# Optimization experiments

Hardware: AMD Instinct MI355X
Metric: run time of the kernel (lower is better)

## Reference

```python
import jax, jax.numpy as jnp
import numpy as np

B, C, F, T = 4, 64, 256, 256
CH = C // 2  # self.n_ch inside the module
EPS = 1e-5


def _cbp(x, W, b, g, be, m, v, a):
    # 1x1 conv == channel matmul, then BatchNorm (inference stats) + PReLU (scalar slope)
    y = jnp.einsum('oi,bift->boft', W, x) + b[None, :, None, None]
    y = (y - m[None, :, None, None]) * jax.lax.rsqrt(v[None, :, None, None] + EPS)
    y = y * g[None, :, None, None] + be[None, :, None, None]
    return jnp.where(y > 0, y, a * y)


def setup_inputs() -> dict:
    key = jax.random.key(0)
    ks = jax.random.split(key, 16)

    def conv_params(i, cin, cout, pre):
        W = jax.random.normal(ks[i], (cout, cin), dtype=jnp.float32) * 0.05
        return {
            pre + '_W': W,
            pre + '_b': jnp.zeros((cout,), jnp.float32),
            pre + '_g': jnp.ones((cout,), jnp.float32),
            pre + '_be': jnp.zeros((cout,), jnp.float32),
            pre + '_m': jax.random.normal(ks[i + 1], (cout,), dtype=jnp.float32) * 0.1,
            pre + '_v': jax.random.uniform(ks[i + 2], (cout,), dtype=jnp.float32) + 0.5,
            pre + '_a': jnp.float32(0.25),
        }

    d = {
        'inp': jax.random.normal(ks[12], (B, C, F, T), dtype=jnp.float32),
        'x': jax.random.normal(ks[13], (B, C, F, T), dtype=jnp.float32),
    }
    d.update(conv_params(0, C, 2 * CH, 'fqk'))
    d.update(conv_params(3, C, CH, 'fv'))
    d.update(conv_params(6, C, 2 * CH, 'tqk'))
    d.update(conv_params(9, CH, C, 'proj'))
    return d


def reference(inp, x,
              fqk_W, fqk_b, fqk_g, fqk_be, fqk_m, fqk_v, fqk_a,
              fv_W, fv_b, fv_g, fv_be, fv_m, fv_v, fv_a,
              tqk_W, tqk_b, tqk_g, tqk_be, tqk_m, tqk_v, tqk_a,
              proj_W, proj_b, proj_g, proj_be, proj_m, proj_v, proj_a):
    scale = 1.0 / jnp.sqrt(jnp.float32(CH))

    # frequency attention
    f_qk = _cbp(inp, fqk_W, fqk_b, fqk_g, fqk_be, fqk_m, fqk_v, fqk_a)  # B,2CH,F,T
    vf = _cbp(x, fv_W, fv_b, fv_g, fv_be, fv_m, fv_v, fv_a)             # B,CH,F,T
    r = f_qk.reshape(f_qk.shape[0], CH, 2, F, T)  # 'b (c k) f t -> b c k f t'
    qf, kf = r[:, :, 0], r[:, :, 1]
    f_score = jnp.einsum('bcft,bcyt->btfy', qf, kf) * scale
    f_score = jax.nn.softmax(f_score, axis=-1)
    fout = jnp.einsum('btfy,bcyt->bcft', f_score, vf)

    # time attention (causal mask)
    t_qk = _cbp(inp, tqk_W, tqk_b, tqk_g, tqk_be, tqk_m, tqk_v, tqk_a)
    r = t_qk.reshape(t_qk.shape[0], CH, 2, F, T)
    qt, kt = r[:, :, 0], r[:, :, 1]
    t_score = jnp.einsum('bcft,bcfy->bfty', qt, kt) * scale
    mask = jnp.triu(jnp.ones((T, T), dtype=bool), k=1)  # j - i + 1 with i == j
    neg = -jnp.finfo(t_score.dtype).max
    t_score = jnp.where(mask, neg, t_score)
    t_score = jax.nn.softmax(t_score, axis=-1)
    tout = jnp.einsum('bfty,bcfy->bcft', t_score, fout)

    out = _cbp(tout, proj_W, proj_b, proj_g, proj_be, proj_m, proj_v, proj_a)
    return out + x
```

## Files before the change

kernel.cpp:

```cpp
#include <hip/hip_runtime.h>
#include <hip/hip_bf16.h>

typedef __hip_bfloat16 bf16;
typedef __attribute__((ext_vector_type(8))) short bf16x8;
typedef __attribute__((ext_vector_type(4))) float f32x4;
typedef __attribute__((ext_vector_type(8))) unsigned short u16x8;
typedef __attribute__((ext_vector_type(4))) unsigned int u32x4;
typedef __attribute__((ext_vector_type(2))) unsigned int u32x2;

struct ConvP {
  const float* W; const float* bi; const float* g; const float* be;
  const float* m; const float* v; const float* a;
};

__device__ __forceinline__ unsigned short f2bf(float f) {
  __hip_bfloat16 h = __float2bfloat16(f);
  return __builtin_bit_cast(unsigned short, h);
}
__device__ __forceinline__ float bf2f(unsigned short u) {
  return __uint_as_float(((unsigned)u) << 16);
}

__global__ __launch_bounds__(256, 2) void conv_qkv(
    const float* __restrict__ inp, const float* __restrict__ x,
    ConvP fqk, ConvP fv, ConvP tqk,
    bf16* __restrict__ Qf, bf16* __restrict__ Kf, bf16* __restrict__ Vf,
    bf16* __restrict__ Qt, bf16* __restrict__ Kt)
{
  __shared__ __attribute__((aligned(16))) unsigned short Xb[64 * 260];
  __shared__ __attribute__((aligned(16))) unsigned short S0[256 * 40];
  __shared__ __attribute__((aligned(16))) unsigned short S1[256 * 40];
  __shared__ __attribute__((aligned(8)))  float2 Pc[160];

  const int tid = threadIdx.x;
  const int b = blockIdx.x >> 8;
  const int f = blockIdx.x & 255;
  const size_t gbase = (size_t)b * 64 * 65536 + f * 256;
  const size_t tbase = (size_t)(b * 256 + f) * 8192;

  const int lane = tid & 63;
  const int wid = tid >> 6;
  const int m16 = lane & 15;
  const int quad = lane >> 4;

  if (tid < 160) {
    const ConvP& P = (tid < 64) ? fqk : (tid < 128) ? tqk : fv;
    const int o = (tid < 64) ? tid : (tid < 128) ? tid - 64 : tid - 128;
    const float A = P.g[o] * rsqrtf(P.v[o] + 1e-5f);
    const float B2 = (P.bi[o] - P.m[o]) * A + P.be[o];
    Pc[tid] = make_float2(A, B2);
  }

  auto load_X = [&](const float* __restrict__ src) {
    #pragma unroll
    for (int r = 0; r < 16; ++r) {
      const int idx = r * 256 + tid;
      const int c = idx >> 6;
      const int t0 = (idx & 63) * 4;
      const float4 v = *(const float4*)(src + gbase + (size_t)c * 65536 + t0);
      unsigned lo = (unsigned)f2bf(v.x) | (((unsigned)f2bf(v.y)) << 16);
      unsigned hi = (unsigned)f2bf(v.z) | (((unsigned)f2bf(v.w)) << 16);
      u32x2 pk = {lo, hi};
      *(u32x2*)&Xb[c * 260 + t0] = pk;
    }
  };

  auto load_A = [&](const float* __restrict__ W, int rowbase, int ks) {
    const float* p = W + (rowbase + m16) * 64 + ks * 32 + quad * 8;
    const float4 lo = *(const float4*)p;
    const float4 hi = *(const float4*)(p + 4);
    bf16x8 r;
    r[0] = (short)f2bf(lo.x); r[1] = (short)f2bf(lo.y);
    r[2] = (short)f2bf(lo.z); r[3] = (short)f2bf(lo.w);
    r[4] = (short)f2bf(hi.x); r[5] = (short)f2bf(hi.y);
    r[6] = (short)f2bf(hi.z); r[7] = (short)f2bf(hi.w);
    return r;
  };

  auto load_B = [&](int tt, int ks) {
    const int t = tt * 16 + m16;
    const int i0 = ks * 32 + quad * 8;
    bf16x8 r;
    #pragma unroll
    for (int j = 0; j < 8; ++j) r[j] = (short)Xb[(i0 + j) * 260 + t];
    return r;
  };

  auto emit = [&](const unsigned short* S, bf16* __restrict__ dst) {
    #pragma unroll
    for (int r = 0; r < 4; ++r) {
      const int chunk = r * 256 + tid;
      const int t = chunk >> 2, part = chunk & 3;
      u32x4 v = *(const u32x4*)&S[t * 40 + part * 8];
      *(u32x4*)(dst + tbase + (size_t)chunk * 8) = v;
    }
  };

  auto leaky = [](float y, float alpha) { return y > 0.f ? y : alpha * y; };

  auto qk_pass = [&](const ConvP& P, int pcb) {
    bf16x8 A[4][2];
    #pragma unroll
    for (int ot = 0; ot < 4; ++ot)
      #pragma unroll
      for (int ks = 0; ks < 2; ++ks) A[ot][ks] = load_A(P.W, ot * 16, ks);
    float pA[4][4], pB[4][4];
    #pragma unroll
    for (int ot = 0; ot < 4; ++ot)
      #pragma unroll
      for (int r = 0; r < 4; ++r) {
        const float2 pp = Pc[pcb + ot * 16 + quad * 4 + r];
        pA[ot][r] = pp.x; pB[ot][r] = pp.y;
      }
    const float alpha = P.a[0];
    #pragma unroll
    for (int i = 0; i < 4; ++i) {
      const int tt = wid * 4 + i;
      const bf16x8 B0 = load_B(tt, 0);
      const bf16x8 B1 = load_B(tt, 1);
      const int t = tt * 16 + m16;
      #pragma unroll
      for (int ot = 0; ot < 4; ++ot) {
        f32x4 acc = {0.f, 0.f, 0.f, 0.f};
        acc = __builtin_amdgcn_mfma_f32_16x16x32_bf16(A[ot][0], B0, acc, 0, 0, 0);
        acc = __builtin_amdgcn_mfma_f32_16x16x32_bf16(A[ot][1], B1, acc, 0, 0, 0);
        float y[4];
        #pragma unroll
        for (int r = 0; r < 4; ++r)
          y[r] = leaky(acc[r] * pA[ot][r] + pB[ot][r], alpha);
        const int ch0 = ot * 8 + quad * 2;
        unsigned q = (unsigned)f2bf(y[0]) | (((unsigned)f2bf(y[2])) << 16);
        unsigned k = (unsigned)f2bf(y[1]) | (((unsigned)f2bf(y[3])) << 16);
        *(unsigned*)&S0[t * 40 + ch0] = q;
        *(unsigned*)&S1[t * 40 + ch0] = k;
      }
    }
  };

  auto v_pass = [&]() {
    bf16x8 A[2][2];
    #pragma unroll
    for (int ot = 0; ot < 2; ++ot)
      #pragma unroll
      for (int ks = 0; ks < 2; ++ks) A[ot][ks] = load_A(fv.W, ot * 16, ks);
    float pA[2][4], pB[2][4];
    #pragma unroll
    for (int ot = 0; ot < 2; ++ot)
      #pragma unroll
      for (int r = 0; r < 4; ++r) {
        const float2 pp = Pc[128 + ot * 16 + quad * 4 + r];
        pA[ot][r] = pp.x; pB[ot][r] = pp.y;
      }
    const float alpha = fv.a[0];
    #pragma unroll
    for (int i = 0; i < 4; ++i) {
      const int tt = wid * 4 + i;
      const bf16x8 B0 = load_B(tt, 0);
      const bf16x8 B1 = load_B(tt, 1);
      const int t = tt * 16 + m16;
      #pragma unroll
      for (int ot = 0; ot < 2; ++ot) {
        f32x4 acc = {0.f, 0.f, 0.f, 0.f};
        acc = __builtin_amdgcn_mfma_f32_16x16x32_bf16(A[ot][0], B0, acc, 0, 0, 0);
        acc = __builtin_amdgcn_mfma_f32_16x16x32_bf16(A[ot][1], B1, acc, 0, 0, 0);
        float y[4];
        #pragma unroll
        for (int r = 0; r < 4; ++r)
          y[r] = leaky(acc[r] * pA[ot][r] + pB[ot][r], alpha);
        const int ch = ot * 16 + quad * 4;
        *(unsigned*)&S0[t * 40 + ch]     = (unsigned)f2bf(y[0]) | (((unsigned)f2bf(y[1])) << 16);
        *(unsigned*)&S0[t * 40 + ch + 2] = (unsigned)f2bf(y[2]) | (((unsigned)f2bf(y[3])) << 16);
      }
    }
  };

  load_X(inp);
  __syncthreads();
  qk_pass(fqk, 0);
  __syncthreads();
  emit(S0, Qf); emit(S1, Kf);
  __syncthreads();
  qk_pass(tqk, 64);
  __syncthreads();
  emit(S0, Qt); emit(S1, Kt);
  __syncthreads();
  load_X(x);
  __syncthreads();
  v_pass();
  __syncthreads();
  emit(S0, Vf);
}

template<bool CAUSAL>
__global__ __launch_bounds__(256) void attn_k(
    const bf16* __restrict__ Qg, const bf16* __restrict__ Kg,
    const bf16* __restrict__ Vg, bf16* __restrict__ Og)
{
  __shared__ __attribute__((aligned(16))) unsigned short Kl[256 * 32];
  __shared__ __attribute__((aligned(16))) unsigned short Vt[32 * 264];
  __shared__ __attribute__((aligned(16))) unsigned short Plds[4][16 * 264];
  __shared__ __attribute__((aligned(16))) unsigned short Wsc[4][512];

  const int inst = blockIdx.x;
  const int b = inst >> 8;
  const int s = inst & 255;
  constexpr int RS = CAUSAL ? 32 : 8192;
  const int qbase = CAUSAL ? inst * 8192 : (b * 2097152 + s * 32);

  const int tid = threadIdx.x;
  #pragma unroll
  for (int k2 = 0; k2 < 4; ++k2) {
    const int chunk = k2 * 256 + tid;
    const int row = chunk >> 2, part = chunk & 3;
    u32x4 val = *(const u32x4*)(Kg + qbase + row * RS + part * 8);
    *(u32x4*)&Kl[row * 32 + part * 8] = val;
  }
  if (tid < 128) {
    const unsigned short* v0 = (const unsigned short*)(Vg + qbase) + (2 * tid) * RS;
    const unsigned short* v1 = v0 + RS;
    u16x8 a[4], c[4];
    #pragma unroll
    for (int q = 0; q < 4; ++q) {
      a[q] = *(const u16x8*)(v0 + 8 * q);
      c[q] = *(const u16x8*)(v1 + 8 * q);
    }
    unsigned int* vt32 = (unsigned int*)Vt;
    #pragma unroll
    for (int cc = 0; cc < 32; ++cc) {
      unsigned lo = a[cc >> 3][cc & 7];
      unsigned hi = c[cc >> 3][cc & 7];
      vt32[(cc * 264 + 2 * tid) >> 1] = lo | (hi << 16);
    }
  }
  __syncthreads();

  const int lane = tid & 63;
  const int wid = tid >> 6;
  const int m16 = lane & 15;
  const int quad = lane >> 4;
  const float sc = 0.17677669529663687f;

  unsigned short* P  = &Plds[wid][0];
  unsigned short* Ws = &Wsc[wid][0];
  const int r4 = lane >> 2, p4 = lane & 3;

  #pragma unroll 1
  for (int it = 0; it < 4; ++it) {
    const int rt = wid + 4 * it;
    {
      u32x4 qv = *(const u32x4*)(Qg + qbase + (rt * 16 + r4) * RS + p4 * 8);
      *(u32x4*)&Ws[r4 * 32 + p4 * 8] = qv;
    }
    const bf16x8 qf = *(const bf16x8*)&Ws[m16 * 32 + quad * 8];
    const int nct = CAUSAL ? (rt + 1) : 16;

    f32x4 acc[16];
    #pragma unroll
    for (int ct = 0; ct < 16; ++ct) {
      if (ct < nct) {
        const bf16x8 kf = *(const bf16x8*)&Kl[(ct * 16 + m16) * 32 + quad * 8];
        f32x4 z = {0.f, 0.f, 0.f, 0.f};
        acc[ct] = __builtin_amdgcn_mfma_f32_16x16x32_bf16(qf, kf, z, 0, 0, 0);
      }
    }
    float mx[4] = {-3e38f, -3e38f, -3e38f, -3e38f};
    #pragma unroll
    for (int ct = 0; ct < 16; ++ct) if (ct < nct) {
      #pragma unroll
      for (int r = 0; r < 4; ++r) {
        float v = acc[ct][r] * sc;
        if (CAUSAL && (ct == nct - 1) && (m16 > quad * 4 + r)) v = -3e38f;
        acc[ct][r] = v;
        mx[r] = fmaxf(mx[r], v);
      }
    }
    #pragma unroll
    for (int r = 0; r < 4; ++r) {
      float m = mx[r];
      #pragma unroll
      for (int d = 1; d < 16; d <<= 1) m = fmaxf(m, __shfl_xor(m, d, 16));
      mx[r] = m;
    }
    float sum[4] = {0.f, 0.f, 0.f, 0.f};
    #pragma unroll
    for (int ct = 0; ct < 16; ++ct) if (ct < nct) {
      #pragma unroll
      for (int r = 0; r < 4; ++r) {
        float p = __expf(acc[ct][r] - mx[r]);
        acc[ct][r] = p;
        sum[r] += p;
      }
    }
    float inv[4];
    #pragma unroll
    for (int r = 0; r < 4; ++r) {
      float ssum = sum[r];
      #pragma unroll
      for (int d = 1; d < 16; d <<= 1) ssum += __shfl_xor(ssum, d, 16);
      inv[r] = 1.0f / ssum;
    }
    #pragma unroll
    for (int ct = 0; ct < 16; ++ct) if (ct < nct) {
      #pragma unroll
      for (int r = 0; r < 4; ++r)
        P[(quad * 4 + r) * 264 + ct * 16 + m16] = f2bf(acc[ct][r] * inv[r]);
    }
    int ksteps = CAUSAL ? ((rt >> 1) + 1) : 8;
    if (CAUSAL && ((rt & 1) == 0)) {
      #pragma unroll
      for (int u = 0; u < 4; ++u) {
        const int e = lane + 64 * u;
        P[(e >> 4) * 264 + (rt + 1) * 16 + (e & 15)] = 0;
      }
    }
    f32x4 o0 = {0.f, 0.f, 0.f, 0.f}, o1 = {0.f, 0.f, 0.f, 0.f};
    #pragma unroll
    for (int ks = 0; ks < 8; ++ks) {
      if (ks < ksteps) {
        const bf16x8 pf  = *(const bf16x8*)&P[m16 * 264 + ks * 32 + quad * 8];
        const bf16x8 vf0 = *(const bf16x8*)&Vt[m16 * 264 + ks * 32 + quad * 8];
        const bf16x8 vf1 = *(const bf16x8*)&Vt[(16 + m16) * 264 + ks * 32 + quad * 8];
        o0 = __builtin_amdgcn_mfma_f32_16x16x32_bf16(pf, vf0, o0, 0, 0, 0);
        o1 = __builtin_amdgcn_mfma_f32_16x16x32_bf16(pf, vf1, o1, 0, 0, 0);
      }
    }
    #pragma unroll
    for (int r = 0; r < 4; ++r) {
      Ws[(quad * 4 + r) * 32 + m16]      = f2bf(o0[r]);
      Ws[(quad * 4 + r) * 32 + 16 + m16] = f2bf(o1[r]);
    }
    {
      u32x4 ov = *(const u32x4*)&Ws[r4 * 32 + p4 * 8];
      *(u32x4*)(Og + qbase + (rt * 16 + r4) * RS + p4 * 8) = ov;
    }
  }
}

__global__ __launch_bounds__(256) void proj_k(
    const bf16* __restrict__ tout, const float* __restrict__ x,
    ConvP pj, float* __restrict__ out)
{
  const int tid = threadIdx.x;
  const int b = blockIdx.x >> 8;
  const int f = blockIdx.x & 255;
  const unsigned short* tp =
      (const unsigned short*)tout + ((b * 256 + f) * 256 + tid) * 32;
  u16x8 tv[4];
  #pragma unroll
  for (int q = 0; q < 4; ++q) tv[q] = *(const u16x8*)(tp + 8 * q);
  float vin[32];
  #pragma unroll
  for (int c = 0; c < 32; ++c) vin[c] = bf2f(tv[c >> 3][c & 7]);
  const float alpha = pj.a[0];
  const int xoff = b * 64 * 65536 + f * 256 + tid;
  #pragma unroll 4
  for (int o = 0; o < 64; ++o) {
    float acc = 0.f;
    #pragma unroll
    for (int i = 0; i < 32; ++i) acc += pj.W[o * 32 + i] * vin[i];
    const float s = rsqrtf(pj.v[o] + 1e-5f);
    const float A = pj.g[o] * s;
    float y = (acc + pj.bi[o] - pj.m[o]) * A + pj.be[o];
    y = y > 0.f ? y : alpha * y;
    out[xoff + o * 65536] = y + x[xoff + o * 65536];
  }
}

extern "C" void kernel_launch(void* const* d_in, const int* in_sizes, int n_in,
                              void* d_out, int out_size, void* d_ws, size_t ws_size,
                              hipStream_t stream) {
  const float* inp = (const float*)d_in[0];
  const float* x   = (const float*)d_in[1];
  auto cp = [&](int i) {
    return ConvP{ (const float*)d_in[i],     (const float*)d_in[i + 1],
                  (const float*)d_in[i + 2], (const float*)d_in[i + 3],
                  (const float*)d_in[i + 4], (const float*)d_in[i + 5],
                  (const float*)d_in[i + 6] };
  };
  ConvP fqk = cp(2), fv = cp(9), tqk = cp(16), pj = cp(23);

  char* ws = (char*)d_ws;
  const size_t SZ = (size_t)4 * 256 * 256 * 32 * 2;
  bf16* Qf = (bf16*)(ws + 0 * SZ);
  bf16* Kf = (bf16*)(ws + 1 * SZ);
  bf16* Vf = (bf16*)(ws + 2 * SZ);
  bf16* Qt = (bf16*)(ws + 3 * SZ);
  bf16* Kt = (bf16*)(ws + 4 * SZ);
  bf16* Ft = (bf16*)(ws + 5 * SZ);
  bf16* To = (bf16*)(ws + 0 * SZ);

  conv_qkv<<<1024, 256, 0, stream>>>(inp, x, fqk, fv, tqk, Qf, Kf, Vf, Qt, Kt);
  attn_k<false><<<1024, 256, 0, stream>>>(Qf, Kf, Vf, Ft);
  attn_k<true><<<1024, 256, 0, stream>>>(Qt, Kt, Ft, To);
  proj_k<<<1024, 256, 0, stream>>>(To, x, pj, (float*)d_out);
}
```

Measured before the change: 355.7 us.

## Fold softmax scale into Q, defer normalization, cache K fragments, MFMA projection

The conv kernel now folds the 1/sqrt(CH)*log2(e) scale into the Q channels' BN affine, so attention can use exp2 directly without a per-score multiply. Softmax normalization moves from the P matrix to the PV output. K fragments are held in registers across row tiles, LDS row strides are padded to 40 to reduce bank conflicts, and attn gets a launch bound of 2 blocks per SM. B fragments are loaded once and reused for both QK passes. The projection kernel is rewritten to use 32x32x16 bf16 MFMA with precomputed BN constants in LDS instead of scalar FMA loops. This adds register pressure from kfr[16] and lowers projection weight precision to bf16.

```diff
diff --git a/kernel.cpp b/kernel.cpp
--- a/kernel.cpp
+++ b/kernel.cpp
@@ -4,6 +4,7 @@
 typedef __hip_bfloat16 bf16;
 typedef __attribute__((ext_vector_type(8))) short bf16x8;
 typedef __attribute__((ext_vector_type(4))) float f32x4;
+typedef __attribute__((ext_vector_type(16))) float f32x16;
 typedef __attribute__((ext_vector_type(8))) unsigned short u16x8;
 typedef __attribute__((ext_vector_type(4))) unsigned int u32x4;
 typedef __attribute__((ext_vector_type(2))) unsigned int u32x2;
@@ -13,12 +14,21 @@
   const float* m; const float* v; const float* a;
 };
 
+#define QS (0.17677669529663687f * 1.4426950408889634f)
+
 __device__ __forceinline__ unsigned short f2bf(float f) {
   __hip_bfloat16 h = __float2bfloat16(f);
   return __builtin_bit_cast(unsigned short, h);
 }
 __device__ __forceinline__ float bf2f(unsigned short u) {
   return __uint_as_float(((unsigned)u) << 16);
+}
+__device__ __forceinline__ float fast_exp2(float x) {
+#if __has_builtin(__builtin_amdgcn_exp2f)
+  return __builtin_amdgcn_exp2f(x);
+#else
+  return exp2f(x);
+#endif
 }
 
 __global__ __launch_bounds__(256, 2) void conv_qkv(
@@ -46,8 +56,9 @@
   if (tid < 160) {
     const ConvP& P = (tid < 64) ? fqk : (tid < 128) ? tqk : fv;
     const int o = (tid < 64) ? tid : (tid < 128) ? tid - 64 : tid - 128;
-    const float A = P.g[o] * rsqrtf(P.v[o] + 1e-5f);
-    const float B2 = (P.bi[o] - P.m[o]) * A + P.be[o];
+    float A = P.g[o] * rsqrtf(P.v[o] + 1e-5f);
+    float B2 = (P.bi[o] - P.m[o]) * A + P.be[o];
+    if (tid < 128 && ((o & 1) == 0)) { A *= QS; B2 *= QS; }
     Pc[tid] = make_float2(A, B2);
   }
 
@@ -98,7 +109,7 @@
 
   auto leaky = [](float y, float alpha) { return y > 0.f ? y : alpha * y; };
 
-  auto qk_pass = [&](const ConvP& P, int pcb) {
+  auto qk_pass = [&](const ConvP& P, int pcb, const bf16x8 (&Bf)[4][2]) {
     bf16x8 A[4][2];
     #pragma unroll
     for (int ot = 0; ot < 4; ++ot)
@@ -115,30 +126,49 @@
     const float alpha = P.a[0];
     #pragma unroll
     for (int i = 0; i < 4; ++i) {
-      const int tt = wid * 4 + i;
-      const bf16x8 B0 = load_B(tt, 0);
-      const bf16x8 B1 = load_B(tt, 1);
-      const int t = tt * 16 + m16;
+      const int t = (wid * 4 + i) * 16 + m16;
       #pragma unroll
       for (int ot = 0; ot < 4; ++ot) {
         f32x4 acc = {0.f, 0.f, 0.f, 0.f};
-        acc = __builtin_amdgcn_mfma_f32_16x16x32_bf16(A[ot][0], B0, acc, 0, 0, 0);
-        acc = __builtin_amdgcn_mfma_f32_16x16x32_bf16(A[ot][1], B1, acc, 0, 0, 0);
+        acc = __builtin_amdgcn_mfma_f32_16x16x32_bf16(A[ot][0], Bf[i][0], acc, 0, 0, 0);
+        acc = __builtin_amdgcn_mfma_f32_16x16x32_bf16(A[ot][1], Bf[i][1], acc, 0, 0, 0);
         float y[4];
         #pragma unroll
         for (int r = 0; r < 4; ++r)
           y[r] = leaky(acc[r] * pA[ot][r] + pB[ot][r], alpha);
         const int ch0 = ot * 8 + quad * 2;
-        unsigned q = (unsigned)f2bf(y[0]) | (((unsigned)f2bf(y[2])) << 16);
-        unsigned k = (unsigned)f2bf(y[1]) | (((unsigned)f2bf(y[3])) << 16);
-        *(unsigned*)&S0[t * 40 + ch0] = q;
-        *(unsigned*)&S1[t * 40 + ch0] = k;
-      }
-    }
-  };
-
-  auto v_pass = [&]() {
-    bf16x8 A[2][2];
+        *(unsigned*)&S0[t * 40 + ch0] = (unsigned)f2bf(y[0]) | (((unsigned)f2bf(y[2])) << 16);
+        *(unsigned*)&S1[t * 40 + ch0] = (unsigned)f2bf(y[1]) | (((unsigned)f2bf(y[3])) << 16);
+      }
+    }
+  };
+
+  load_X(inp);
+  __syncthreads();
+
+  bf16x8 Bf[4][2];
+  #pragma unroll
+  for (int i = 0; i < 4; ++i)
+    #pragma unroll
+    for (int ks = 0; ks < 2; ++ks) Bf[i][ks] = load_B(wid * 4 + i, ks);
+
+  qk_pass(fqk, 0, Bf);
+  __syncthreads();
+  emit(S0, Qf); emit(S1, Kf);
+  __syncthreads();
+  qk_pass(tqk, 64, Bf);
+  __syncthreads();
+  emit(S0, Qt); emit(S1, Kt);
+  __syncthreads();
+  load_X(x);
+  __syncthreads();
+
+  {
+    bf16x8 A[2][2], Bv[4][2];
+    #pragma unroll
+    for (int i = 0; i < 4; ++i)
+      #pragma unroll
+      for (int ks = 0; ks < 2; ++ks) Bv[i][ks] = load_B(wid * 4 + i, ks);
     #pragma unroll
     for (int ot = 0; ot < 2; ++ot)
       #pragma unroll
@@ -154,15 +184,12 @@
     const float alpha = fv.a[0];
     #pragma unroll
     for (int i = 0; i < 4; ++i) {
-      const int tt = wid * 4 + i;
-      const bf16x8 B0 = load_B(tt, 0);
-      const bf16x8 B1 = load_B(tt, 1);
-      const int t = tt * 16 + m16;
+      const int t = (wid * 4 + i) * 16 + m16;
       #pragma unroll
       for (int ot = 0; ot < 2; ++ot) {
         f32x4 acc = {0.f, 0.f, 0.f, 0.f};
-        acc = __builtin_amdgcn_mfma_f32_16x16x32_bf16(A[ot][0], B0, acc, 0, 0, 0);
-        acc = __builtin_amdgcn_mfma_f32_16x16x32_bf16(A[ot][1], B1, acc, 0, 0, 0);
+        acc = __builtin_amdgcn_mfma_f32_16x16x32_bf16(A[ot][0], Bv[i][0], acc, 0, 0, 0);
+        acc = __builtin_amdgcn_mfma_f32_16x16x32_bf16(A[ot][1], Bv[i][1], acc, 0, 0, 0);
         float y[4];
         #pragma unroll
         for (int r = 0; r < 4; ++r)
@@ -172,34 +199,20 @@
         *(unsigned*)&S0[t * 40 + ch + 2] = (unsigned)f2bf(y[2]) | (((unsigned)f2bf(y[3])) << 16);
       }
     }
-  };
-
-  load_X(inp);
-  __syncthreads();
-  qk_pass(fqk, 0);
-  __syncthreads();
-  emit(S0, Qf); emit(S1, Kf);
-  __syncthreads();
-  qk_pass(tqk, 64);
-  __syncthreads();
-  emit(S0, Qt); emit(S1, Kt);
-  __syncthreads();
-  load_X(x);
-  __syncthreads();
-  v_pass();
+  }
   __syncthreads();
   emit(S0, Vf);
 }
 
 template<bool CAUSAL>
-__global__ __launch_bounds__(256) void attn_k(
+__global__ __launch_bounds__(256, 2) void attn_k(
     const bf16* __restrict__ Qg, const bf16* __restrict__ Kg,
     const bf16* __restrict__ Vg, bf16* __restrict__ Og)
 {
-  __shared__ __attribute__((aligned(16))) unsigned short Kl[256 * 32];
+  __shared__ __attribute__((aligned(16))) unsigned short Kl[256 * 40];
   __shared__ __attribute__((aligned(16))) unsigned short Vt[32 * 264];
   __shared__ __attribute__((aligned(16))) unsigned short Plds[4][16 * 264];
-  __shared__ __attribute__((aligned(16))) unsigned short Wsc[4][512];
+  __shared__ __attribute__((aligned(16))) unsigned short Wsc[4][16 * 40];
 
   const int inst = blockIdx.x;
   const int b = inst >> 8;
@@ -213,7 +226,7 @@
     const int chunk = k2 * 256 + tid;
     const int row = chunk >> 2, part = chunk & 3;
     u32x4 val = *(const u32x4*)(Kg + qbase + row * RS + part * 8);
-    *(u32x4*)&Kl[row * 32 + part * 8] = val;
+    *(u32x4*)&Kl[row * 40 + part * 8] = val;
   }
   if (tid < 128) {
     const unsigned short* v0 = (const unsigned short*)(Vg + qbase) + (2 * tid) * RS;
@@ -238,29 +251,32 @@
   const int wid = tid >> 6;
   const int m16 = lane & 15;
   const int quad = lane >> 4;
-  const float sc = 0.17677669529663687f;
 
   unsigned short* P  = &Plds[wid][0];
   unsigned short* Ws = &Wsc[wid][0];
   const int r4 = lane >> 2, p4 = lane & 3;
+
+  bf16x8 kfr[16];
+  #pragma unroll
+  for (int ct = 0; ct < 16; ++ct)
+    kfr[ct] = *(const bf16x8*)&Kl[(ct * 16 + m16) * 40 + quad * 8];
 
   #pragma unroll 1
   for (int it = 0; it < 4; ++it) {
     const int rt = wid + 4 * it;
     {
       u32x4 qv = *(const u32x4*)(Qg + qbase + (rt * 16 + r4) * RS + p4 * 8);
-      *(u32x4*)&Ws[r4 * 32 + p4 * 8] = qv;
-    }
-    const bf16x8 qf = *(const bf16x8*)&Ws[m16 * 32 + quad * 8];
+      *(u32x4*)&Ws[r4 * 40 + p4 * 8] = qv;
+    }
+    const bf16x8 qf = *(const bf16x8*)&Ws[m16 * 40 + quad * 8];
     const int nct = CAUSAL ? (rt + 1) : 16;
 
     f32x4 acc[16];
     #pragma unroll
     for (int ct = 0; ct < 16; ++ct) {
       if (ct < nct) {
-        const bf16x8 kf = *(const bf16x8*)&Kl[(ct * 16 + m16) * 32 + quad * 8];
         f32x4 z = {0.f, 0.f, 0.f, 0.f};
-        acc[ct] = __builtin_amdgcn_mfma_f32_16x16x32_bf16(qf, kf, z, 0, 0, 0);
+        acc[ct] = __builtin_amdgcn_mfma_f32_16x16x32_bf16(qf, kfr[ct], z, 0, 0, 0);
       }
     }
     float mx[4] = {-3e38f, -3e38f, -3e38f, -3e38f};
@@ -268,7 +284,7 @@
     for (int ct = 0; ct < 16; ++ct) if (ct < nct) {
       #pragma unroll
       for (int r = 0; r < 4; ++r) {
-        float v = acc[ct][r] * sc;
+        float v = acc[ct][r];
         if (CAUSAL && (ct == nct - 1) && (m16 > quad * 4 + r)) v = -3e38f;
         acc[ct][r] = v;
         mx[r] = fmaxf(mx[r], v);
@@ -286,7 +302,7 @@
     for (int ct = 0; ct < 16; ++ct) if (ct < nct) {
       #pragma unroll
       for (int r = 0; r < 4; ++r) {
-        float p = __expf(acc[ct][r] - mx[r]);
+        float p = fast_exp2(acc[ct][r] - mx[r]);
         acc[ct][r] = p;
         sum[r] += p;
       }
@@ -303,7 +319,7 @@
     for (int ct = 0; ct < 16; ++ct) if (ct < nct) {
       #pragma unroll
       for (int r = 0; r < 4; ++r)
-        P[(quad * 4 + r) * 264 + ct * 16 + m16] = f2bf(acc[ct][r] * inv[r]);
+        P[(quad * 4 + r) * 264 + ct * 16 + m16] = f2bf(acc[ct][r]);
     }
     int ksteps = CAUSAL ? ((rt >> 1) + 1) : 8;
     if (CAUSAL && ((rt & 1) == 0)) {
@@ -326,11 +342,11 @@
     }
     #pragma unroll
     for (int r = 0; r < 4; ++r) {
-      Ws[(quad * 4 + r) * 32 + m16]      = f2bf(o0[r]);
-      Ws[(quad * 4 + r) * 32 + 16 + m16] = f2bf(o1[r]);
+      Ws[(quad * 4 + r) * 40 + m16]      = f2bf(o0[r] * inv[r]);
+      Ws[(quad * 4 + r) * 40 + 16 + m16] = f2bf(o1[r] * inv[r]);
     }
     {
-      u32x4 ov = *(const u32x4*)&Ws[r4 * 32 + p4 * 8];
+      u32x4 ov = *(const u32x4*)&Ws[r4 * 40 + p4 * 8];
       *(u32x4*)(Og + qbase + (rt * 16 + r4) * RS + p4 * 8) = ov;
     }
   }
@@ -340,29 +356,61 @@
     const bf16* __restrict__ tout, const float* __restrict__ x,
     ConvP pj, float* __restrict__ out)
 {
+  __shared__ float2 Pc[64];
   const int tid = threadIdx.x;
   const int b = blockIdx.x >> 8;
   const int f = blockIdx.x & 255;
-  const unsigned short* tp =
-      (const unsigned short*)tout + ((b * 256 + f) * 256 + tid) * 32;
-  u16x8 tv[4];
+  if (tid < 64) {
+    const float A = pj.g[tid] * rsqrtf(pj.v[tid] + 1e-5f);
+    const float B2 = (pj.bi[tid] - pj.m[tid]) * A + pj.be[tid];
+    Pc[tid] = make_float2(A, B2);
+  }
+  const int lane = tid & 63;
+  const int wid = tid >> 6;
+  const int n32 = lane & 31;
+  const int h = lane >> 5;
+
+  bf16x8 Afr[2][2];
   #pragma unroll
-  for (int q = 0; q < 4; ++q) tv[q] = *(const u16x8*)(tp + 8 * q);
-  float vin[32];
+  for (int ot = 0; ot < 2; ++ot)
+    #pragma unroll
+    for (int ks = 0; ks < 2; ++ks) {
+      const float* p = pj.W + (ot * 32 + n32) * 32 + ks * 16 + h * 8;
+      const float4 lo = *(const float4*)p;
+      const float4 hi = *(const float4*)(p + 4);
+      bf16x8 r;
+      r[0] = (short)f2bf(lo.x); r[1] = (short)f2bf(lo.y);
+      r[2] = (short)f2bf(lo.z); r[3] = (short)f2bf(lo.w);
+      r[4] = (short)f2bf(hi.x); r[5] = (short)f2bf(hi.y);
+      r[6] = (short)f2bf(hi.z); r[7] = (short)f2bf(hi.w);
+      Afr[ot][ks] = r;
+    }
+  __syncthreads();
+
+  const float alpha = pj.a[0];
+  const size_t gbase = (size_t)b * 64 * 65536 + f * 256;
+  const size_t tbase = (size_t)(b * 256 + f) * 8192;
+
   #pragma unroll
-  for (int c = 0; c < 32; ++c) vin[c] = bf2f(tv[c >> 3][c & 7]);
-  const float alpha = pj.a[0];
-  const int xoff = b * 64 * 65536 + f * 256 + tid;
-  #pragma unroll 4
-  for (int o = 0; o < 64; ++o) {
-    float acc = 0.f;
-    #pragma unroll
-    for (int i = 0; i < 32; ++i) acc += pj.W[o * 32 + i] * vin[i];
-    const float s = rsqrtf(pj.v[o] + 1e-5f);
-    const float A = pj.g[o] * s;
-    float y = (acc + pj.bi[o] - pj.m[o]) * A + pj.be[o];
-    y = y > 0.f ? y : alpha * y;
-    out[xoff + o * 65536] = y + x[xoff + o * 65536];
+  for (int tt = 0; tt < 2; ++tt) {
+    const int t = wid * 64 + tt * 32 + n32;
+    const bf16x8 B0 = *(const bf16x8*)(tout + tbase + (size_t)t * 32 + 0 * 16 + h * 8);
+    const bf16x8 B1 = *(const bf16x8*)(tout + tbase + (size_t)t * 32 + 1 * 16 + h * 8);
+    #pragma unroll
+    for (int ot = 0; ot < 2; ++ot) {
+      f32x16 acc = {};
+      acc = __builtin_amdgcn_mfma_f32_32x32x16_bf16(Afr[ot][0], B0, acc, 0, 0, 0);
+      acc = __builtin_amdgcn_mfma_f32_32x32x16_bf16(Afr[ot][1], B1, acc, 0, 0, 0);
+      #pragma unroll
+      for (int reg = 0; reg < 16; ++reg) {
+        const int o = ot * 32 + (reg & 3) + 8 * (reg >> 2) + 4 * h;
+        const float2 pp = Pc[o];
+        float y = acc[reg] * pp.x + pp.y;
+        y = y > 0.f ? y : alpha * y;
+        const size_t off = gbase + (size_t)o * 65536 + t;
+        out[off] = y + x[off];
+      }
+    }
   }
 }
 
```

Result: faster. 327.8 us (-7.9%).
